# Kernel optimization log

Hardware: AMD Instinct MI355X
Metric: run time of the kernel (lower is better)

The kernel has to match this reference:

```python
import jax, jax.numpy as jnp
import numpy as np


def setup_inputs() -> dict:
    key = jax.random.key(0)
    ks = jax.random.split(key, 6)
    b, t, k, h = 8, 128, 128, 4
    q_x = jax.random.normal(ks[0], (b, t, k), dtype=jnp.float32)
    kv_x = jax.random.normal(ks[1], (b, t, t - 1, k), dtype=jnp.float32)
    s = 1.0 / np.sqrt(k).astype(np.float32)
    Wk = jax.random.normal(ks[2], (k, k), dtype=jnp.float32) * s  # tokeys.weight
    Wq = jax.random.normal(ks[3], (k, k), dtype=jnp.float32) * s  # toqueries.weight
    Wv = jax.random.normal(ks[4], ((1 + k) * h, 2 * k), dtype=jnp.float32) * (1.0 / np.sqrt(2 * k).astype(np.float32))  # tovalues.weight
    bv = jax.random.normal(ks[5], ((1 + k) * h,), dtype=jnp.float32) * 0.01  # tovalues.bias
    return dict(q_x=q_x, kv_x=kv_x, Wk=Wk, Wq=Wq, Wv=Wv, bv=bv)


def reference(q_x, kv_x, Wk, Wq, Wv, bv):
    # kv_x: (b, t, t-1, k); q_x: (b, t, k)
    b, t, m, k = kv_x.shape  # m == t - 1
    h = Wv.shape[0] // (k + 1)
    # torch Linear: y = x @ W.T
    keys = jnp.einsum('btmk,jk->btmj', kv_x, Wk)          # (b,t,m,k)
    queries = jnp.einsum('btk,jk->btj', q_x, Wq)          # (b,t,k)
    queries = jnp.broadcast_to(queries[:, :, None, :], (b, t, m, k))
    value_input = jnp.concatenate([keys, queries], axis=-1)  # (b,t,m,2k)
    vals = jnp.einsum('btmc,oc->btmo', value_input, Wv) + bv  # (b,t,m,(1+k)h)
    vals = vals.reshape(b, t, m, h, k + 1)
    score = vals[..., 0]        # (b,t,m,h)
    values = vals[..., 1:]      # (b,t,m,h,k)
    w = jax.nn.softmax(score, axis=2)  # softmax over the t-1 (pair) axis
    x = jnp.einsum('btmh,btmhk->bthk', w, values)  # weighted sum over pairs
    return x.reshape(b, t, h * k)
```

## Files before the change

### kernel.cpp

```cpp
#include <hip/hip_runtime.h>

#define KD 128
#define NH 4
#define MM 127
#define NO 516

#define OFF_W1S 0
#define OFF_WC  512
#define OFF_C   (512 + 131072)

__global__ void precompute_w(const float* __restrict__ Wk,
                             const float* __restrict__ Wq,
                             const float* __restrict__ Wv,
                             float* __restrict__ ws) {
    int o = blockIdx.x;
    int k = threadIdx.x;
    const float* wvrow = Wv + o * 256;
    float acc1 = 0.f, acc2 = 0.f;
    #pragma unroll 8
    for (int j = 0; j < 128; ++j) {
        acc1 += wvrow[j]       * Wk[j * 128 + k];
        acc2 += wvrow[128 + j] * Wq[j * 128 + k];
    }
    int h = o / 129;
    int r = o - h * 129;
    if (r == 0) {
        ws[OFF_W1S + h * 128 + k] = acc1;
    } else {
        int dd = r - 1;
        ws[OFF_WC + (size_t)(h * 256 + k) * 128 + dd]       = acc1;
        ws[OFF_WC + (size_t)(h * 256 + 128 + k) * 128 + dd] = acc2;
    }
}

__global__ __launch_bounds__(256, 4)
void attn_bt(const float* __restrict__ kv_x, float* __restrict__ ws) {
    __shared__ float ssc[512];
    __shared__ float swt[512];
    __shared__ float cpart[8][512];

    const int bt  = blockIdx.x;
    const int tid = threadIdx.x;
    const int dq  = tid & 31;
    const int g   = tid >> 5;

    float4 w1s[NH];
    #pragma unroll
    for (int h = 0; h < NH; ++h)
        w1s[h] = *(const float4*)(ws + OFF_W1S + h * KD + dq * 4);

    const float4* src = (const float4*)(kv_x + (size_t)bt * MM * KD);
    const int bit4 = (tid >> 4) & 1;
    const int bit3 = (tid >> 3) & 1;
    const int myh  = bit4 * 2 + bit3;

    float4 cur = src[g * 32 + dq];
    float4 nxt = src[(g + 8) * 32 + dq];
    #pragma unroll
    for (int k = 0; k < 16; ++k) {
        int mp = g + 8 * (k + 2);
        float4 pre = make_float4(0.f, 0.f, 0.f, 0.f);
        if (k < 14 && mp < MM) pre = src[mp * 32 + dq];
        int m = g + 8 * k;
        float4 v = cur;
        float p0 = v.x*w1s[0].x + v.y*w1s[0].y + v.z*w1s[0].z + v.w*w1s[0].w;
        float p1 = v.x*w1s[1].x + v.y*w1s[1].y + v.z*w1s[1].z + v.w*w1s[1].w;
        float p2 = v.x*w1s[2].x + v.y*w1s[2].y + v.z*w1s[2].z + v.w*w1s[2].w;
        float p3 = v.x*w1s[3].x + v.y*w1s[3].y + v.z*w1s[3].z + v.w*w1s[3].w;
        float x = bit4 ? p0 : p2;
        float y = bit4 ? p1 : p3;
        float a = (bit4 ? p2 : p0) + __shfl_xor(x, 16);
        float b = (bit4 ? p3 : p1) + __shfl_xor(y, 16);
        float z = bit3 ? a : b;
        float vr = (bit3 ? b : a) + __shfl_xor(z, 8);
        vr += __shfl_xor(vr, 4);
        vr += __shfl_xor(vr, 2);
        vr += __shfl_xor(vr, 1);
        if ((tid & 7) == 0 && m < MM) ssc[m * 4 + myh] = vr;
        cur = nxt; nxt = pre;
    }
    __syncthreads();

    {
        int h = tid >> 6, lane = tid & 63;
        float v0 = ssc[lane * 4 + h];
        bool has1 = (lane + 64) < MM;
        float v1 = has1 ? ssc[(lane + 64) * 4 + h] : -1e30f;
        float mx = fmaxf(v0, v1);
        #pragma unroll
        for (int off = 32; off; off >>= 1) mx = fmaxf(mx, __shfl_xor(mx, off));
        float e0 = __expf(v0 - mx);
        float e1 = has1 ? __expf(v1 - mx) : 0.f;
        float s = e0 + e1;
        #pragma unroll
        for (int off = 32; off; off >>= 1) s += __shfl_xor(s, off);
        float inv = 1.f / s;
        swt[lane * 4 + h] = e0 * inv;
        swt[(lane + 64) * 4 + h] = has1 ? e1 * inv : 0.f;
    }
    __syncthreads();

    float4 c0 = make_float4(0.f,0.f,0.f,0.f);
    float4 c1 = make_float4(0.f,0.f,0.f,0.f);
    float4 c2 = make_float4(0.f,0.f,0.f,0.f);
    float4 c3 = make_float4(0.f,0.f,0.f,0.f);
    #pragma unroll
    for (int k = 0; k < 16; ++k) {
        int m = g + 8 * k;
        if (m < MM) {
            float4 kq = src[m * 32 + dq];
            float4 w4 = *(const float4*)&swt[m * 4];
            c0.x += w4.x*kq.x; c0.y += w4.x*kq.y; c0.z += w4.x*kq.z; c0.w += w4.x*kq.w;
            c1.x += w4.y*kq.x; c1.y += w4.y*kq.y; c1.z += w4.y*kq.z; c1.w += w4.y*kq.w;
            c2.x += w4.z*kq.x; c2.y += w4.z*kq.y; c2.z += w4.z*kq.z; c2.w += w4.z*kq.w;
            c3.x += w4.w*kq.x; c3.y += w4.w*kq.y; c3.z += w4.w*kq.z; c3.w += w4.w*kq.w;
        }
    }
    *(float4*)&cpart[g][0 * KD + dq * 4] = c0;
    *(float4*)&cpart[g][1 * KD + dq * 4] = c1;
    *(float4*)&cpart[g][2 * KD + dq * 4] = c2;
    *(float4*)&cpart[g][3 * KD + dq * 4] = c3;
    __syncthreads();

    float* cdst = ws + OFF_C + (size_t)bt * 512;
    #pragma unroll
    for (int rep = 0; rep < 2; ++rep) {
        int o = tid + rep * 256;
        float s = 0.f;
        #pragma unroll
        for (int gg = 0; gg < 8; ++gg) s += cpart[gg][o];
        cdst[o] = s;
    }
}

#define BM 32
#define BN 64
#define BK 64
#define AP 34
#define BP 68

__global__ __launch_bounds__(256, 2)
void proj_out(const float* __restrict__ q_x,
              const float* __restrict__ bv,
              const float* __restrict__ ws,
              float* __restrict__ out) {
    __shared__ float sAT[BK][AP];
    __shared__ float sB[BK][BP];

    const int r0  = blockIdx.x * BM;
    const int dd0 = blockIdx.y * BN;
    const int h   = blockIdx.z;
    const int tid = threadIdx.x;
    const int tx  = tid & 15;
    const int ty  = tid >> 4;
    const float* cmat = ws + OFF_C;
    const float* Wct  = ws + OFF_WC;

    float acc[2][4];
    #pragma unroll
    for (int i = 0; i < 2; ++i)
        #pragma unroll
        for (int j = 0; j < 4; ++j) acc[i][j] = 0.f;

    for (int ks = 0; ks < 4; ++ks) {
        int kk0 = ks * BK;
        const float* Abase; int Astride;
        if (kk0 < 128) { Abase = cmat + h * KD + kk0; Astride = 512; }
        else           { Abase = q_x + (kk0 - 128);   Astride = KD;  }
        #pragma unroll
        for (int i = 0; i < 2; ++i) {
            int idx = tid + i * 256;
            int r = idx >> 4, c4 = idx & 15;
            float4 v = *(const float4*)(Abase + (size_t)(r0 + r) * Astride + c4 * 4);
            sAT[c4 * 4 + 0][r] = v.x;
            sAT[c4 * 4 + 1][r] = v.y;
            sAT[c4 * 4 + 2][r] = v.z;
            sAT[c4 * 4 + 3][r] = v.w;
        }
        #pragma unroll
        for (int i = 0; i < 4; ++i) {
            int idx = tid + i * 256;
            int c = idx >> 4, d4 = idx & 15;
            *(float4*)&sB[c][d4 * 4] =
                *(const float4*)(Wct + (size_t)(h * 256 + kk0 + c) * 128 + dd0 + d4 * 4);
        }
        __syncthreads();
        #pragma unroll 8
        for (int c = 0; c < BK; ++c) {
            float2 a  = *(const float2*)&sAT[c][ty * 2];
            float4 b4 = *(const float4*)&sB[c][tx * 4];
            acc[0][0] += a.x * b4.x; acc[0][1] += a.x * b4.y;
            acc[0][2] += a.x * b4.z; acc[0][3] += a.x * b4.w;
            acc[1][0] += a.y * b4.x; acc[1][1] += a.y * b4.y;
            acc[1][2] += a.y * b4.z; acc[1][3] += a.y * b4.w;
        }
        __syncthreads();
    }
    float bb[4];
    #pragma unroll
    for (int j = 0; j < 4; ++j) bb[j] = bv[h * 129 + 1 + dd0 + tx * 4 + j];
    #pragma unroll
    for (int i = 0; i < 2; ++i) {
        float4 v;
        v.x = acc[i][0] + bb[0];
        v.y = acc[i][1] + bb[1];
        v.z = acc[i][2] + bb[2];
        v.w = acc[i][3] + bb[3];
        *(float4*)(out + (size_t)(r0 + ty * 2 + i) * 512 + h * KD + dd0 + tx * 4) = v;
    }
}

extern "C" void kernel_launch(void* const* d_in, const int* in_sizes, int n_in,
                              void* d_out, int out_size, void* d_ws, size_t ws_size,
                              hipStream_t stream) {
    const float* q_x  = (const float*)d_in[0];
    const float* kv_x = (const float*)d_in[1];
    const float* Wk   = (const float*)d_in[2];
    const float* Wq   = (const float*)d_in[3];
    const float* Wv   = (const float*)d_in[4];
    const float* bv   = (const float*)d_in[5];
    float* out = (float*)d_out;
    float* ws  = (float*)d_ws;

    int bt = in_sizes[0] / KD;

    hipLaunchKernelGGL(precompute_w, dim3(NO), dim3(128), 0, stream, Wk, Wq, Wv, ws);
    hipLaunchKernelGGL(attn_bt, dim3(bt), dim3(256), 0, stream, kv_x, ws);
    hipLaunchKernelGGL(proj_out, dim3(bt / BM, KD / BN, NH), dim3(256), 0, stream,
                       q_x, bv, ws, out);
}
```

Before: 42.30 us.

## Split score computation into a grid-stride streaming kernel before softmax/aggregation

Moves the per-pair score dot products out of the per-(b,t) attention kernel into a separate grid-stride kernel that streams all kv_x rows and writes scores to workspace. The attention kernel then reads the precomputed scores, does the softmax and the weighted sum. The goal is better memory-level parallelism and bandwidth for the first pass over kv_x, which previously ran with one block per row group. The cost is an extra kernel launch, a score buffer round-trip through global memory, and kv_x being read twice in separate kernels, where the second read may not hit cache.

```diff
diff --git a/kernel.cpp b/kernel.cpp
--- a/kernel.cpp
+++ b/kernel.cpp
@@ -4,10 +4,12 @@
 #define NH 4
 #define MM 127
 #define NO 516
+#define NROWS (1024 * MM)
 
 #define OFF_W1S 0
 #define OFF_WC  512
-#define OFF_C   (512 + 131072)
+#define OFF_S   (512 + 131072)
+#define OFF_C   (512 + 131072 + 520192)
 
 __global__ void precompute_w(const float* __restrict__ Wk,
                              const float* __restrict__ Wq,
@@ -34,35 +36,30 @@
 }
 
 __global__ __launch_bounds__(256, 4)
-void attn_bt(const float* __restrict__ kv_x, float* __restrict__ ws) {
-    __shared__ float ssc[512];
-    __shared__ float swt[512];
-    __shared__ float cpart[8][512];
-
-    const int bt  = blockIdx.x;
-    const int tid = threadIdx.x;
-    const int dq  = tid & 31;
-    const int g   = tid >> 5;
+void scores_stream(const float* __restrict__ kv_x, float* __restrict__ ws) {
+    const int tid  = threadIdx.x;
+    const int dq   = tid & 31;
+    const int lane = tid & 63;
 
     float4 w1s[NH];
     #pragma unroll
     for (int h = 0; h < NH; ++h)
         w1s[h] = *(const float4*)(ws + OFF_W1S + h * KD + dq * 4);
 
-    const float4* src = (const float4*)(kv_x + (size_t)bt * MM * KD);
     const int bit4 = (tid >> 4) & 1;
     const int bit3 = (tid >> 3) & 1;
     const int myh  = bit4 * 2 + bit3;
 
-    float4 cur = src[g * 32 + dq];
-    float4 nxt = src[(g + 8) * 32 + dq];
-    #pragma unroll
-    for (int k = 0; k < 16; ++k) {
-        int mp = g + 8 * (k + 2);
-        float4 pre = make_float4(0.f, 0.f, 0.f, 0.f);
-        if (k < 14 && mp < MM) pre = src[mp * 32 + dq];
-        int m = g + 8 * k;
-        float4 v = cur;
+    const float4* src = (const float4*)kv_x;
+    float* S = ws + OFF_S;
+
+    const int wid    = (blockIdx.x * 256 + tid) >> 6;
+    const int nwaves = gridDim.x * 4;
+    const int NP     = NROWS / 2;
+
+    for (int p = wid; p < NP; p += nwaves) {
+        float4 v = src[(size_t)p * 64 + lane];
+        int R = 2 * p + (lane >> 5);
         float p0 = v.x*w1s[0].x + v.y*w1s[0].y + v.z*w1s[0].z + v.w*w1s[0].w;
         float p1 = v.x*w1s[1].x + v.y*w1s[1].y + v.z*w1s[1].z + v.w*w1s[1].w;
         float p2 = v.x*w1s[2].x + v.y*w1s[2].y + v.z*w1s[2].z + v.w*w1s[2].w;
@@ -76,16 +73,26 @@
         vr += __shfl_xor(vr, 4);
         vr += __shfl_xor(vr, 2);
         vr += __shfl_xor(vr, 1);
-        if ((tid & 7) == 0 && m < MM) ssc[m * 4 + myh] = vr;
-        cur = nxt; nxt = pre;
-    }
-    __syncthreads();
+        if ((tid & 7) == 0) S[(size_t)R * 4 + myh] = vr;
+    }
+}
+
+__global__ __launch_bounds__(256, 4)
+void attn_sc(const float* __restrict__ kv_x, float* __restrict__ ws) {
+    __shared__ float swt[512];
+    __shared__ float cpart[8][512];
+
+    const int bt  = blockIdx.x;
+    const int tid = threadIdx.x;
+    const int dq  = tid & 31;
+    const int g   = tid >> 5;
 
     {
         int h = tid >> 6, lane = tid & 63;
-        float v0 = ssc[lane * 4 + h];
+        const float* S = ws + OFF_S + (size_t)bt * MM * 4;
+        float v0 = S[lane * 4 + h];
         bool has1 = (lane + 64) < MM;
-        float v1 = has1 ? ssc[(lane + 64) * 4 + h] : -1e30f;
+        float v1 = has1 ? S[(lane + 64) * 4 + h] : -1e30f;
         float mx = fmaxf(v0, v1);
         #pragma unroll
         for (int off = 32; off; off >>= 1) mx = fmaxf(mx, __shfl_xor(mx, off));
@@ -100,6 +107,7 @@
     }
     __syncthreads();
 
+    const float4* src = (const float4*)(kv_x + (size_t)bt * MM * KD);
     float4 c0 = make_float4(0.f,0.f,0.f,0.f);
     float4 c1 = make_float4(0.f,0.f,0.f,0.f);
     float4 c2 = make_float4(0.f,0.f,0.f,0.f);
@@ -225,7 +233,8 @@
     int bt = in_sizes[0] / KD;
 
     hipLaunchKernelGGL(precompute_w, dim3(NO), dim3(128), 0, stream, Wk, Wq, Wv, ws);
-    hipLaunchKernelGGL(attn_bt, dim3(bt), dim3(256), 0, stream, kv_x, ws);
+    hipLaunchKernelGGL(scores_stream, dim3(2048), dim3(256), 0, stream, kv_x, ws);
+    hipLaunchKernelGGL(attn_sc, dim3(bt), dim3(256), 0, stream, kv_x, ws);
     hipLaunchKernelGGL(proj_out, dim3(bt / BM, KD / BN, NH), dim3(256), 0, stream,
                        q_x, bv, ws, out);
 }
```

Measured after the change: 47.23 us. +11.7%, slower.
